# Kernel optimization log

Measured on AMD Instinct MI355X. Metric: run time of the kernel, lower is better.

## Reference

```python
import jax, jax.numpy as jnp
import numpy as np


def setup_inputs() -> dict:
    key = jax.random.key(0)
    ks = jax.random.split(key, 5)
    B, S, D = 4, 2048, 768
    scale = 0.02  # keep pre-softmax scores in a sane range
    return {
        "x": jax.random.normal(ks[0], (B, S, D), dtype=jnp.float32),
        "wq": jax.random.normal(ks[1], (D, D), dtype=jnp.float32) * scale,
        "wk": jax.random.normal(ks[2], (D, D), dtype=jnp.float32) * scale,
        "wv": jax.random.normal(ks[3], (D, D), dtype=jnp.float32) * scale,
        "wo": jax.random.normal(ks[4], (D, D), dtype=jnp.float32) * scale,
    }


NUM_HEADS = 12
NEG = -1000000000.0


def reference(x, wq, wk, wv, wo):
    B, S, D = x.shape
    H = NUM_HEADS
    dh = D // H
    # nn.Linear(bias=False): y = x @ W.T ; split heads -> [B, H, S, dh]
    def proj(w):
        return (x @ w.T).reshape(B, S, H, dh).transpose(0, 2, 1, 3)
    q, k, v = proj(wq), proj(wk), proj(wv)
    # scores [B, H, S, S] with causal mask (strict upper triangle gets -1e9 added)
    score = jnp.einsum("bhqd,bhkd->bhqk", q, k) / jnp.float32(np.sqrt(dh))
    causal = jnp.triu(jnp.ones((S, S), dtype=bool), k=1)
    score = score + jnp.where(causal, jnp.float32(NEG), jnp.float32(0.0))
    attn = jax.nn.softmax(score, axis=-1)
    out = jnp.einsum("bhqk,bhkd->bhqd", attn, v)
    out = out.transpose(0, 2, 1, 3).reshape(B, S, D)
    return out @ wo.T
```

## Files before the change

### kernel.cpp

```cpp
#include <hip/hip_runtime.h>
#include <stdint.h>

typedef unsigned short u16;
typedef __attribute__((ext_vector_type(8))) short short8;
typedef __attribute__((ext_vector_type(4))) short s16x4;
typedef __attribute__((ext_vector_type(4))) float f32x4;
typedef __attribute__((ext_vector_type(2))) unsigned uint2v;

#define MFMA16(a, b, c) __builtin_amdgcn_mfma_f32_16x16x32_bf16(a, b, c, 0, 0, 0)

#if __has_builtin(__builtin_amdgcn_mfma_f32_16x16x16bf16_1k)
__device__ __forceinline__ f32x4 pv_mfma(s16x4 a, s16x4 b, f32x4 c) {
  return __builtin_amdgcn_mfma_f32_16x16x16bf16_1k(a, b, c, 0, 0, 0);
}
#else
__device__ __forceinline__ f32x4 pv_mfma(s16x4 a, s16x4 b, f32x4 c) {
  asm volatile("v_mfma_f32_16x16x16_bf16 %0, %1, %2, %0" : "+v"(c) : "v"(a), "v"(b));
  return c;
}
#endif

__device__ __forceinline__ void async16(void* lds, const void* g) {
  __builtin_amdgcn_global_load_lds(
      (const __attribute__((address_space(1))) void*)g,
      (__attribute__((address_space(3))) void*)lds, 16, 0, 0);
}

__device__ __forceinline__ u16 f2bf(float f) {
  unsigned u = __float_as_uint(f);
  u += 0x7FFF + ((u >> 16) & 1);
  return (u16)(u >> 16);
}

__device__ __forceinline__ unsigned cvtpk(float lo, float hi) {
  unsigned r;
  asm("v_cvt_pk_bf16_f32 %0, %1, %2" : "=v"(r) : "v"(lo), "v"(hi));
  return r;
}

#define QSCALE 0.18033688011112042f
#define MASKV -30000.0f

__global__ void convert_x(const float* __restrict__ src, u16* __restrict__ dst) {
  int i = blockIdx.x * 256 + threadIdx.x;
  float4 v = ((const float4*)src)[i];
  unsigned lo = (unsigned)f2bf(v.x) | ((unsigned)f2bf(v.y) << 16);
  unsigned hi = (unsigned)f2bf(v.z) | ((unsigned)f2bf(v.w) << 16);
  ((uint2*)dst)[i] = make_uint2(lo, hi);
}

__global__ void convert_w(const float* __restrict__ wq, const float* __restrict__ wk,
                          const float* __restrict__ wv, const float* __restrict__ wo,
                          u16* __restrict__ wqkv, u16* __restrict__ wob) {
  int i = blockIdx.x * 256 + threadIdx.x;
  int wsel = i / 147456;
  int r = i - wsel * 147456;
  const float* s = (wsel == 0) ? wq : (wsel == 1) ? wk : (wsel == 2) ? wv : wo;
  float4 v = ((const float4*)s)[r];
  unsigned lo = (unsigned)f2bf(v.x) | ((unsigned)f2bf(v.y) << 16);
  unsigned hi = (unsigned)f2bf(v.z) | ((unsigned)f2bf(v.w) << 16);
  uint2 w = make_uint2(lo, hi);
  if (wsel < 3) ((uint2*)wqkv)[wsel * 147456 + r] = w;
  else ((uint2*)wob)[r] = w;
}

template <int MODE>
__global__ __launch_bounds__(256) void gemm_bt(const u16* __restrict__ A,
                                               const u16* __restrict__ Bw,
                                               u16* __restrict__ Qb, u16* __restrict__ Kb,
                                               u16* __restrict__ Vb, float* __restrict__ Out) {
  __shared__ __align__(16) u16 As[2][128 * 32];
  __shared__ __align__(16) u16 Bs[2][128 * 32];
  const int bm = blockIdx.x & 63;
  const int bn = blockIdx.x >> 6;
  const int tid = threadIdx.x;
  const int wave = tid >> 6, lane = tid & 63;
  const int arow = lane & 15, kg = lane >> 4;
  const int wr = wave >> 1, wc = wave & 1;

  const int o = tid * 16;
  const int rowS = o >> 6;
  const int cbS = o & 63;
  const char* gA0 = (const char*)A + (size_t)(bm * 128 + rowS) * 1536 + cbS;
  const char* gA1 = gA0 + (size_t)64 * 1536;
  const char* gB0 = (const char*)Bw + (size_t)(bn * 128 + rowS) * 1536 + cbS;
  const char* gB1 = gB0 + (size_t)64 * 1536;
  const int ldsw = wave * 1024;

  f32x4 acc[4][4];
#pragma unroll
  for (int m = 0; m < 4; ++m)
#pragma unroll
    for (int n = 0; n < 4; ++n) acc[m][n] = (f32x4)(0.0f);

  auto stage = [&](int buf) {
    async16((char*)As + buf * 8192 + ldsw,        gA0);
    async16((char*)As + buf * 8192 + ldsw + 4096, gA1);
    async16((char*)Bs + buf * 8192 + ldsw,        gB0);
    async16((char*)Bs + buf * 8192 + ldsw + 4096, gB1);
    gA0 += 64; gA1 += 64; gB0 += 64; gB1 += 64;
  };

  stage(0);
  asm volatile("s_waitcnt vmcnt(0)" ::: "memory");
  __builtin_amdgcn_s_barrier();

  int cur = 0;
  for (int kk = 0; kk < 24; ++kk) {
    if (kk + 1 < 24) stage(cur ^ 1);

    const char* Ac = (const char*)As + cur * 8192;
    const char* Bc = (const char*)Bs + cur * 8192;
    short8 av[4], bv[4];
#pragma unroll
    for (int m = 0; m < 4; ++m)
      av[m] = *(const short8*)(Ac + (wr * 64 + m * 16 + arow) * 64 + kg * 16);
#pragma unroll
    for (int n = 0; n < 4; ++n)
      bv[n] = *(const short8*)(Bc + (wc * 64 + n * 16 + arow) * 64 + kg * 16);
#pragma unroll
    for (int m = 0; m < 4; ++m)
#pragma unroll
      for (int n = 0; n < 4; ++n) acc[m][n] = MFMA16(av[m], bv[n], acc[m][n]);

    asm volatile("s_waitcnt vmcnt(0)" ::: "memory");
    __builtin_amdgcn_s_barrier();
    cur ^= 1;
  }

  if (MODE == 0) {
    const int b = bm >> 4;
    const int sb = (bm & 15) * 128 + wr * 64 + kg * 4;
    const int which = bn / 6;
    const int cbase = bn * 128 - which * 768 + wc * 64;
    if (which == 2) {
#pragma unroll
      for (int n = 0; n < 4; ++n) {
        int hc = cbase + n * 16 + arow;
        size_t rowb = ((size_t)(b * 12 + (hc >> 6)) * 64 + (hc & 63)) * 2048;
#pragma unroll
        for (int m = 0; m < 4; ++m) {
          uint2v w;
          w.x = cvtpk(acc[m][n][0], acc[m][n][1]);
          w.y = cvtpk(acc[m][n][2], acc[m][n][3]);
          *(uint2v*)(Vb + rowb + sb + m * 16) = w;
        }
      }
    } else {
      u16* const dst = which ? Kb : Qb;
      const float sc = which ? 1.0f : QSCALE;
#pragma unroll
      for (int n = 0; n < 4; ++n) {
        int hc = cbase + n * 16 + arow;
        size_t hb = ((size_t)(b * 12 + (hc >> 6)) * 2048) * 64 + (hc & 63);
#pragma unroll
        for (int m = 0; m < 4; ++m)
#pragma unroll
          for (int i = 0; i < 4; ++i)
            dst[hb + (size_t)(sb + m * 16 + i) * 64] = f2bf(acc[m][n][i] * sc);
      }
    }
  } else {
    const int rbase = bm * 128 + wr * 64 + kg * 4;
#pragma unroll
    for (int m = 0; m < 4; ++m)
#pragma unroll
      for (int n = 0; n < 4; ++n) {
        const int c = bn * 128 + wc * 64 + n * 16 + arow;
#pragma unroll
        for (int i = 0; i < 4; ++i)
          Out[(size_t)(rbase + m * 16 + i) * 768 + c] = acc[m][n][i];
      }
  }
}

__global__ __launch_bounds__(256) void attn_kernel(const u16* __restrict__ Qb,
                                                   const u16* __restrict__ Kb,
                                                   const u16* __restrict__ Vb,
                                                   u16* __restrict__ AOb) {
  __shared__ __align__(16) u16 Ks[2][64 * 64];
  __shared__ __align__(16) u16 Vt[2][64 * 64];

  const int bid = blockIdx.x;
  const int qt = 31 - (bid / 48);
  const int bh = bid % 48;
  const int tid = threadIdx.x, wave = tid >> 6, lane = tid & 63;
  const int arow = lane & 15, kg = lane >> 4;
  const size_t hbase = (size_t)bh * (2048 * 64);
  const u16* Qh = Qb + hbase;
  const int q0 = qt * 64 + wave * 16;

  short8 qf[2];
#pragma unroll
  for (int ks = 0; ks < 2; ++ks)
    qf[ks] = *(const short8*)(Qh + (size_t)(q0 + arow) * 64 + ks * 32 + kg * 8);

  f32x4 o_acc[4];
#pragma unroll
  for (int n = 0; n < 4; ++n) o_acc[n] = (f32x4)(0.0f);
  float mrow = MASKV, lrow = 0.0f;

  const int o0 = tid * 16;
  const int r0 = o0 >> 7, cb0 = o0 & 127;
  const int r1 = r0 + 32;
  const int sw0 = cb0 ^ (((r0 ^ (r0 >> 3)) & 7) << 4);
  const int sw1 = cb0 ^ (((r1 ^ (r1 >> 3)) & 7) << 4);
  char* const KsB = (char*)Ks;
  char* const VtB = (char*)Vt;
  const int ldsw = wave * 1024;

  const char* gK0 = (const char*)(Kb + hbase) + r0 * 128 + sw0;
  const char* gK1 = (const char*)(Kb + hbase) + r1 * 128 + sw1;
  const char* gV0 = (const char*)(Vb + hbase) + (size_t)r0 * 4096 + sw0;
  const char* gV1 = (const char*)(Vb + hbase) + (size_t)r1 * 4096 + sw1;

  const int ktiles = qt + 1;

  auto stage = [&](int buf) {
    async16(KsB + buf * 8192 + ldsw,        gK0);
    async16(KsB + buf * 8192 + ldsw + 4096, gK1);
    async16(VtB + buf * 8192 + ldsw,        gV0);
    async16(VtB + buf * 8192 + ldsw + 4096, gV1);
    gK0 += 8192; gK1 += 8192; gV0 += 128; gV1 += 128;
  };

  stage(0);
  asm volatile("s_waitcnt vmcnt(0)" ::: "memory");
  __builtin_amdgcn_s_barrier();

  int cur = 0;
  for (int kt = 0; kt < ktiles; ++kt) {
    if (kt + 1 < ktiles) stage(cur ^ 1);

    const char* Kc = KsB + cur * 8192;
    const char* Vc = VtB + cur * 8192;

    f32x4 s_acc[4];
#pragma unroll
    for (int cg = 0; cg < 4; ++cg) s_acc[cg] = (f32x4)(0.0f);
#pragma unroll
    for (int cg = 0; cg < 4; ++cg) {
      int krow = cg * 16 + arow;
      int fsw = ((krow ^ (krow >> 3)) & 7) << 4;
#pragma unroll
      for (int ks = 0; ks < 2; ++ks) {
        short8 kf = *(const short8*)(Kc + (krow << 7) + ((ks * 64 + kg * 16) ^ fsw));
        s_acc[cg] = MFMA16(kf, qf[ks], s_acc[cg]);
      }
    }

    if (kt == ktiles - 1) {
      int rel = wave * 16 + arow - kg * 4;
#pragma unroll
      for (int cg = 0; cg < 4; ++cg)
#pragma unroll
        for (int i = 0; i < 4; ++i)
          s_acc[cg][i] = (cg * 16 + i > rel) ? MASKV : s_acc[cg][i];
    }

    float rmax = s_acc[0][0];
#pragma unroll
    for (int cg = 0; cg < 4; ++cg)
#pragma unroll
      for (int i = 0; i < 4; ++i) rmax = fmaxf(rmax, s_acc[cg][i]);
    rmax = fmaxf(rmax, __shfl_xor(rmax, 16));
    rmax = fmaxf(rmax, __shfl_xor(rmax, 32));

    {
      float mnew = fmaxf(mrow, rmax);
      float corr = exp2f(mrow - mnew);
      mrow = mnew;
      lrow *= corr;
#pragma unroll
      for (int n = 0; n < 4; ++n)
#pragma unroll
        for (int i = 0; i < 4; ++i) o_acc[n][i] *= corr;
    }

    float p[4][4];
    float rs = 0.0f;
#pragma unroll
    for (int cg = 0; cg < 4; ++cg)
#pragma unroll
      for (int i = 0; i < 4; ++i) {
        float e = exp2f(s_acc[cg][i] - mrow);
        p[cg][i] = e;
        rs += e;
      }
    rs += __shfl_xor(rs, 16);
    rs += __shfl_xor(rs, 32);
    lrow += rs;

    s16x4 pb[4];
#pragma unroll
    for (int cg = 0; cg < 4; ++cg) {
      uint2v w;
      w.x = cvtpk(p[cg][0], p[cg][1]);
      w.y = cvtpk(p[cg][2], p[cg][3]);
      pb[cg] = __builtin_bit_cast(s16x4, w);
    }

#pragma unroll
    for (int n = 0; n < 4; ++n) {
      int vrow = n * 16 + arow;
      int f2 = ((vrow ^ (vrow >> 3)) & 7) << 4;
      const char* vb0 = Vc + (vrow << 7);
#pragma unroll
      for (int cg = 0; cg < 4; ++cg) {
        s16x4 va = *(const s16x4*)(vb0 + ((cg * 32 + kg * 8) ^ f2));
        o_acc[n] = pv_mfma(va, pb[cg], o_acc[n]);
      }
    }

    asm volatile("s_waitcnt vmcnt(0)" ::: "memory");
    __builtin_amdgcn_s_barrier();
    cur ^= 1;
  }

  const int b = bh / 12, h = bh - b * 12;
  float rinv = 1.0f / lrow;
  size_t obase = ((size_t)b * 2048 + q0 + arow) * 768 + h * 64 + kg * 4;
#pragma unroll
  for (int n = 0; n < 4; ++n) {
#pragma unroll
    for (int t = 0; t < 2; ++t) {
      unsigned w = cvtpk(o_acc[n][2 * t] * rinv, o_acc[n][2 * t + 1] * rinv);
      *(unsigned*)(&AOb[obase + n * 16 + 2 * t]) = w;
    }
  }
}

extern "C" void kernel_launch(void* const* d_in, const int* in_sizes, int n_in,
                              void* d_out, int out_size, void* d_ws, size_t ws_size,
                              hipStream_t stream) {
  const float* x = (const float*)d_in[0];
  const float* wq = (const float*)d_in[1];
  const float* wk = (const float*)d_in[2];
  const float* wv = (const float*)d_in[3];
  const float* wo = (const float*)d_in[4];
  float* out = (float*)d_out;

  char* ws = (char*)d_ws;
  u16* xb   = (u16*)(ws);
  u16* wqkv = (u16*)(ws + 12582912);
  u16* wob  = (u16*)(ws + 16121856);
  u16* Qb   = (u16*)(ws + 17301504);
  u16* Kb   = (u16*)(ws + 29884416);
  u16* Vb   = (u16*)(ws + 42467328);
  u16* AOb  = (u16*)(ws + 55050240);

  convert_x<<<6144, 256, 0, stream>>>(x, xb);
  convert_w<<<2304, 256, 0, stream>>>(wq, wk, wv, wo, wqkv, wob);

  gemm_bt<0><<<64 * 18, 256, 0, stream>>>(xb, wqkv, Qb, Kb, Vb, nullptr);
  attn_kernel<<<48 * 32, 256, 0, stream>>>(Qb, Kb, Vb, AOb);
  gemm_bt<1><<<64 * 6, 256, 0, stream>>>(AOb, wob, nullptr, nullptr, nullptr, out);
}
```

Measured before the change: 140.6 us.

## Pair complementary causal query tiles in one 512-thread attention block sharing K/V

After: 279.2 us. 98.6% more time.

```diff
diff --git a/kernel.cpp b/kernel.cpp
--- a/kernel.cpp
+++ b/kernel.cpp
@@ -174,21 +174,23 @@
   }
 }
 
-__global__ __launch_bounds__(256) void attn_kernel(const u16* __restrict__ Qb,
-                                                   const u16* __restrict__ Kb,
-                                                   const u16* __restrict__ Vb,
-                                                   u16* __restrict__ AOb) {
+__global__ __launch_bounds__(512, 8) void attn_kernel(const u16* __restrict__ Qb,
+                                                      const u16* __restrict__ Kb,
+                                                      const u16* __restrict__ Vb,
+                                                      u16* __restrict__ AOb) {
   __shared__ __align__(16) u16 Ks[2][64 * 64];
   __shared__ __align__(16) u16 Vt[2][64 * 64];
 
   const int bid = blockIdx.x;
-  const int qt = 31 - (bid / 48);
+  const int p = bid / 48;
   const int bh = bid % 48;
   const int tid = threadIdx.x, wave = tid >> 6, lane = tid & 63;
+  const int wgrp = wave >> 2, wq = wave & 3;
   const int arow = lane & 15, kg = lane >> 4;
+  const int qt = wgrp ? p : (31 - p);
   const size_t hbase = (size_t)bh * (2048 * 64);
   const u16* Qh = Qb + hbase;
-  const int q0 = qt * 64 + wave * 16;
+  const int q0 = qt * 64 + wq * 16;
 
   short8 qf[2];
 #pragma unroll
@@ -202,118 +204,114 @@
 
   const int o0 = tid * 16;
   const int r0 = o0 >> 7, cb0 = o0 & 127;
-  const int r1 = r0 + 32;
   const int sw0 = cb0 ^ (((r0 ^ (r0 >> 3)) & 7) << 4);
-  const int sw1 = cb0 ^ (((r1 ^ (r1 >> 3)) & 7) << 4);
   char* const KsB = (char*)Ks;
   char* const VtB = (char*)Vt;
-  const int ldsw = wave * 1024;
-
-  const char* gK0 = (const char*)(Kb + hbase) + r0 * 128 + sw0;
-  const char* gK1 = (const char*)(Kb + hbase) + r1 * 128 + sw1;
-  const char* gV0 = (const char*)(Vb + hbase) + (size_t)r0 * 4096 + sw0;
-  const char* gV1 = (const char*)(Vb + hbase) + (size_t)r1 * 4096 + sw1;
-
-  const int ktiles = qt + 1;
+  const int ldsw = wave << 10;
+
+  const char* gK = (const char*)(Kb + hbase) + r0 * 128 + sw0;
+  const char* gV = (const char*)(Vb + hbase) + (size_t)r0 * 4096 + sw0;
+
+  const int nt = 32 - p;
 
   auto stage = [&](int buf) {
-    async16(KsB + buf * 8192 + ldsw,        gK0);
-    async16(KsB + buf * 8192 + ldsw + 4096, gK1);
-    async16(VtB + buf * 8192 + ldsw,        gV0);
-    async16(VtB + buf * 8192 + ldsw + 4096, gV1);
-    gK0 += 8192; gK1 += 8192; gV0 += 128; gV1 += 128;
+    async16(KsB + buf * 8192 + ldsw, gK);
+    async16(VtB + buf * 8192 + ldsw, gV);
+    gK += 8192;
+    gV += 128;
   };
 
+  const int rel = wq * 16 + arow - kg * 4;
+
   stage(0);
-  asm volatile("s_waitcnt vmcnt(0)" ::: "memory");
-  __builtin_amdgcn_s_barrier();
+  __syncthreads();
 
   int cur = 0;
-  for (int kt = 0; kt < ktiles; ++kt) {
-    if (kt + 1 < ktiles) stage(cur ^ 1);
-
-    const char* Kc = KsB + cur * 8192;
-    const char* Vc = VtB + cur * 8192;
-
-    f32x4 s_acc[4];
-#pragma unroll
-    for (int cg = 0; cg < 4; ++cg) s_acc[cg] = (f32x4)(0.0f);
-#pragma unroll
-    for (int cg = 0; cg < 4; ++cg) {
-      int krow = cg * 16 + arow;
-      int fsw = ((krow ^ (krow >> 3)) & 7) << 4;
-#pragma unroll
-      for (int ks = 0; ks < 2; ++ks) {
-        short8 kf = *(const short8*)(Kc + (krow << 7) + ((ks * 64 + kg * 16) ^ fsw));
-        s_acc[cg] = MFMA16(kf, qf[ks], s_acc[cg]);
+  for (int kt = 0; kt < nt; ++kt) {
+    if (kt + 1 < nt) stage(cur ^ 1);
+
+    if (kt <= qt) {
+      const char* Kc = KsB + cur * 8192;
+      const char* Vc = VtB + cur * 8192;
+
+      f32x4 s_acc[4];
+#pragma unroll
+      for (int cg = 0; cg < 4; ++cg) s_acc[cg] = (f32x4)(0.0f);
+#pragma unroll
+      for (int cg = 0; cg < 4; ++cg) {
+        int krow = cg * 16 + arow;
+        int fsw = ((krow ^ (krow >> 3)) & 7) << 4;
+#pragma unroll
+        for (int ks = 0; ks < 2; ++ks) {
+          short8 kf = *(const short8*)(Kc + (krow << 7) + ((ks * 64 + kg * 16) ^ fsw));
+          s_acc[cg] = MFMA16(kf, qf[ks], s_acc[cg]);
+        }
+      }
+
+      if (kt == qt) {
+#pragma unroll
+        for (int cg = 0; cg < 4; ++cg)
+#pragma unroll
+          for (int i = 0; i < 4; ++i)
+            s_acc[cg][i] = (cg * 16 + i > rel) ? MASKV : s_acc[cg][i];
+      }
+
+      float rmax = s_acc[0][0];
+#pragma unroll
+      for (int cg = 0; cg < 4; ++cg)
+#pragma unroll
+        for (int i = 0; i < 4; ++i) rmax = fmaxf(rmax, s_acc[cg][i]);
+      rmax = fmaxf(rmax, __shfl_xor(rmax, 16));
+      rmax = fmaxf(rmax, __shfl_xor(rmax, 32));
+
+      {
+        float mnew = fmaxf(mrow, rmax);
+        float corr = exp2f(mrow - mnew);
+        mrow = mnew;
+        lrow *= corr;
+#pragma unroll
+        for (int n = 0; n < 4; ++n)
+#pragma unroll
+          for (int i = 0; i < 4; ++i) o_acc[n][i] *= corr;
+      }
+
+      float pv[4][4];
+      float rs = 0.0f;
+#pragma unroll
+      for (int cg = 0; cg < 4; ++cg)
+#pragma unroll
+        for (int i = 0; i < 4; ++i) {
+          float e = exp2f(s_acc[cg][i] - mrow);
+          pv[cg][i] = e;
+          rs += e;
+        }
+      rs += __shfl_xor(rs, 16);
+      rs += __shfl_xor(rs, 32);
+      lrow += rs;
+
+      s16x4 pb[4];
+#pragma unroll
+      for (int cg = 0; cg < 4; ++cg) {
+        uint2v w;
+        w.x = cvtpk(pv[cg][0], pv[cg][1]);
+        w.y = cvtpk(pv[cg][2], pv[cg][3]);
+        pb[cg] = __builtin_bit_cast(s16x4, w);
+      }
+
+#pragma unroll
+      for (int n = 0; n < 4; ++n) {
+        int vrow = n * 16 + arow;
+        int f2 = ((vrow ^ (vrow >> 3)) & 7) << 4;
+        const char* vb0 = Vc + (vrow << 7);
+#pragma unroll
+        for (int cg = 0; cg < 4; ++cg) {
+          s16x4 va = *(const s16x4*)(vb0 + ((cg * 32 + kg * 8) ^ f2));
+          o_acc[n] = pv_mfma(va, pb[cg], o_acc[n]);
+        }
       }
     }
 
-    if (kt == ktiles - 1) {
-      int rel = wave * 16 + arow - kg * 4;
-#pragma unroll
-      for (int cg = 0; cg < 4; ++cg)
-#pragma unroll
-        for (int i = 0; i < 4; ++i)
-          s_acc[cg][i] = (cg * 16 + i > rel) ? MASKV : s_acc[cg][i];
-    }
-
-    float rmax = s_acc[0][0];
-#pragma unroll
-    for (int cg = 0; cg < 4; ++cg)
-#pragma unroll
-      for (int i = 0; i < 4; ++i) rmax = fmaxf(rmax, s_acc[cg][i]);
-    rmax = fmaxf(rmax, __shfl_xor(rmax, 16));
-    rmax = fmaxf(rmax, __shfl_xor(rmax, 32));
-
-    {
-      float mnew = fmaxf(mrow, rmax);
-      float corr = exp2f(mrow - mnew);
-      mrow = mnew;
-      lrow *= corr;
-#pragma unroll
-      for (int n = 0; n < 4; ++n)
-#pragma unroll
-        for (int i = 0; i < 4; ++i) o_acc[n][i] *= corr;
-    }
-
-    float p[4][4];
-    float rs = 0.0f;
-#pragma unroll
-    for (int cg = 0; cg < 4; ++cg)
-#pragma unroll
-      for (int i = 0; i < 4; ++i) {
-        float e = exp2f(s_acc[cg][i] - mrow);
-        p[cg][i] = e;
-        rs += e;
-      }
-    rs += __shfl_xor(rs, 16);
-    rs += __shfl_xor(rs, 32);
-    lrow += rs;
-
-    s16x4 pb[4];
-#pragma unroll
-    for (int cg = 0; cg < 4; ++cg) {
-      uint2v w;
-      w.x = cvtpk(p[cg][0], p[cg][1]);
-      w.y = cvtpk(p[cg][2], p[cg][3]);
-      pb[cg] = __builtin_bit_cast(s16x4, w);
-    }
-
-#pragma unroll
-    for (int n = 0; n < 4; ++n) {
-      int vrow = n * 16 + arow;
-      int f2 = ((vrow ^ (vrow >> 3)) & 7) << 4;
-      const char* vb0 = Vc + (vrow << 7);
-#pragma unroll
-      for (int cg = 0; cg < 4; ++cg) {
-        s16x4 va = *(const s16x4*)(vb0 + ((cg * 32 + kg * 8) ^ f2));
-        o_acc[n] = pv_mfma(va, pb[cg], o_acc[n]);
-      }
-    }
-
-    asm volatile("s_waitcnt vmcnt(0)" ::: "memory");
-    __builtin_amdgcn_s_barrier();
+    __syncthreads();
     cur ^= 1;
   }
 
@@ -353,6 +351,6 @@
   convert_w<<<2304, 256, 0, stream>>>(wq, wk, wv, wo, wqkv, wob);
 
   gemm_bt<0><<<64 * 18, 256, 0, stream>>>(xb, wqkv, Qb, Kb, Vb, nullptr);
-  attn_kernel<<<48 * 32, 256, 0, stream>>>(Qb, Kb, Vb, AOb);
+  attn_kernel<<<48 * 16, 512, 0, stream>>>(Qb, Kb, Vb, AOb);
   gemm_bt<1><<<64 * 6, 256, 0, stream>>>(AOb, wob, nullptr, nullptr, nullptr, out);
 }
```
